# Performance work log

Measured on AMD Instinct MI355X. Metric: run time of the kernel, lower is better.

## Reference

```python
import jax, jax.numpy as jnp
import numpy as np

B, T, D, H, C = 64, 2048, 320, 256, 10  # batch, seq, input, hidden, classes


def _lstm_layer(x, W_ih, W_hh, b_ih, b_hh):
    """Single LSTM layer, batch_first x: [B,T,Din] -> [B,T,H].
    PyTorch gate order: i, f, g, o."""
    # Precompute input projections for all timesteps at once (big GEMM, efficient)
    xg = jnp.einsum('btd,gd->btg', x, W_ih) + b_ih + b_hh  # [B,T,4H]
    Hh = W_hh.shape[1]

    def step(carry, xt):
        h, c = carry
        g = xt + h @ W_hh.T  # [B,4H]
        i, f, gg, o = jnp.split(g, 4, axis=-1)
        i = jax.nn.sigmoid(i)
        f = jax.nn.sigmoid(f)
        gg = jnp.tanh(gg)
        o = jax.nn.sigmoid(o)
        c = f * c + i * gg
        h = o * jnp.tanh(c)
        return (h, c), h

    h0 = jnp.zeros((x.shape[0], Hh), x.dtype)
    (_, _), hs = jax.lax.scan(step, (h0, h0), jnp.swapaxes(xg, 0, 1))
    return jnp.swapaxes(hs, 0, 1)  # [B,T,H]


def setup_inputs() -> dict:
    key = jax.random.key(0)
    ks = jax.random.split(key, 12)
    s_ih0 = 1.0 / np.sqrt(H)
    inp = {
        'x': jax.random.normal(ks[0], (B, T, D), dtype=jnp.float32),
        'W_ih0': jax.random.uniform(ks[1], (4 * H, D), jnp.float32, -s_ih0, s_ih0),
        'W_hh0': jax.random.uniform(ks[2], (4 * H, H), jnp.float32, -s_ih0, s_ih0),
        'b_ih0': jax.random.uniform(ks[3], (4 * H,), jnp.float32, -s_ih0, s_ih0),
        'b_hh0': jax.random.uniform(ks[4], (4 * H,), jnp.float32, -s_ih0, s_ih0),
        'W_ih1': jax.random.uniform(ks[5], (4 * H, H), jnp.float32, -s_ih0, s_ih0),
        'W_hh1': jax.random.uniform(ks[6], (4 * H, H), jnp.float32, -s_ih0, s_ih0),
        'b_ih1': jax.random.uniform(ks[7], (4 * H,), jnp.float32, -s_ih0, s_ih0),
        'b_hh1': jax.random.uniform(ks[8], (4 * H,), jnp.float32, -s_ih0, s_ih0),
        'W_fc': jax.random.uniform(ks[9], (C, H), jnp.float32, -s_ih0, s_ih0),
        'b_fc': jax.random.uniform(ks[10], (C,), jnp.float32, -s_ih0, s_ih0),
    }
    return inp


def reference(x, W_ih0, W_hh0, b_ih0, b_hh0, W_ih1, W_hh1, b_ih1, b_hh1, W_fc, b_fc):
    h1 = _lstm_layer(x, W_ih0, W_hh0, b_ih0, b_hh0)   # [B,T,H]
    h2 = _lstm_layer(h1, W_ih1, W_hh1, b_ih1, b_hh1)  # [B,T,H]
    last = h2[:, -1, :]                                # output[:, -1, :]
    return last @ W_fc.T + b_fc                        # [B,C]
```

## Files before the change

### kernel.cpp

```cpp
#include <hip/hip_runtime.h>
#include <stdint.h>

typedef __bf16 bf16x8 __attribute__((ext_vector_type(8)));
typedef float f32x4 __attribute__((ext_vector_type(4)));
typedef unsigned long long u64;

#define BB 64
#define TT 2048
#define DD 320
#define HH 256
#define NC 10
#define GH 1024

#define GB 4
#define GJ 4
#define MB 16
#define JW 64
#define NTHREADS 512
#define SHS 264
#define SGS 260
#define NPAIR 2048
#define NPT 4
#define NRW 3
#define NWG_LAUNCH 64
#define HSROUNDS 3
#define HSSPIN 256

__device__ __forceinline__ unsigned short f2bf(float f) {
  unsigned u = __float_as_uint(f);
  u += 0x7FFF + ((u >> 16) & 1);
  return (unsigned short)(u >> 16);
}

__global__ void convert_bf16_k(const float* __restrict__ src,
                               unsigned short* __restrict__ dst, int n) {
  int i = blockIdx.x * blockDim.x + threadIdx.x;
  int st = gridDim.x * blockDim.x;
  for (; i < n; i += st) dst[i] = f2bf(src[i]);
}

__global__ void bias_sum_k(const float* __restrict__ a, const float* __restrict__ b,
                           float* __restrict__ d, int n) {
  int i = blockIdx.x * blockDim.x + threadIdx.x;
  if (i < n) d[i] = a[i] + b[i];
}

__global__ void zero_claim_k(int* p) { p[threadIdx.x] = 0; }

__device__ __forceinline__ float sigm(float x) { return 1.f / (1.f + __expf(-x)); }
__device__ __forceinline__ float tanh_s(float x) { return 2.f * sigm(2.f * x) - 1.f; }

__device__ __forceinline__ u64 ald(const u64* p) {
  return __hip_atomic_load(p, __ATOMIC_RELAXED, __HIP_MEMORY_SCOPE_AGENT);
}
__device__ __forceinline__ void ast(u64* p, u64 v) {
  __hip_atomic_store(p, v, __ATOMIC_RELAXED, __HIP_MEMORY_SCOPE_AGENT);
}

__device__ __forceinline__ void st_wt(u64* p, u64 v) {
  asm volatile("global_store_dwordx2 %0, %1, off" : : "v"(p), "v"(v) : "memory");
}
__device__ __forceinline__ void ld_sc0_issue(const u64* p, u64& d) {
  asm volatile("global_load_dwordx2 %0, %1, off sc0" : "=&v"(d) : "v"(p) : "memory");
}
__device__ __forceinline__ u64 ld1_sc0(const u64* p) {
  u64 v;
  asm volatile("global_load_dwordx2 %0, %1, off sc0\n\t"
               "s_waitcnt vmcnt(0)"
               : "=&v"(v) : "v"(p) : "memory");
  __builtin_amdgcn_sched_barrier(0);
  return v;
}
__device__ __forceinline__ void vm_wait0() {
  asm volatile("s_waitcnt vmcnt(0)" ::: "memory");
  __builtin_amdgcn_sched_barrier(0);
}

template <int KCX, bool IS_L0>
__device__ __forceinline__ void lstm_role(
    const unsigned short* __restrict__ xin,
    const u64* __restrict__ xtag,
    const unsigned short* __restrict__ Wih,
    const unsigned short* __restrict__ Whh,
    const float* __restrict__ bias,
    u64* __restrict__ h1out,
    float* __restrict__ hlast,
    u64* __restrict__ hx,
    unsigned short* sX, unsigned short* sH, float* sG,
    int gb, int gj, bool local)
{
  constexpr int KX = KCX * 32;
  constexpr int KCH = HH / 32;

  const int tid = threadIdx.x;
  const int wv = tid >> 6;
  const int ln = tid & 63;
  const int lm = ln & 15;
  const int lq = ln >> 4;
  const int j0 = gj * JW;
  const int b0 = gb * MB;

  bf16x8 bW[2][KCX + KCH];
  float bsv[2];
#pragma unroll
  for (int i = 0; i < 2; ++i) {
    int r = (wv * 2 + i) * 16 + lm;
    int grow = (r >> 6) * HH + j0 + (r & 63);
#pragma unroll
    for (int kc = 0; kc < KCX; ++kc)
      bW[i][kc] = *(const bf16x8*)&Wih[(size_t)grow * KX + kc * 32 + lq * 8];
#pragma unroll
    for (int kc = 0; kc < KCH; ++kc)
      bW[i][KCX + kc] = *(const bf16x8*)&Whh[(size_t)grow * HH + kc * 32 + lq * 8];
    bsv[i] = bias[grow];
  }

  int rw[NRW];
#pragma unroll
  for (int i = 0; i < NRW; ++i) {
    int rp = i * NTHREADS + tid;
    int em = rp / 96;
    int q = rp - em * 96;
    int pe = q >> 5;
    pe += (pe >= gj);
    rw[i] = em * 128 + pe * 32 + (q & 31);
  }

  u64* const hxg = hx + (size_t)gb * 2 * NPAIR;
  unsigned* const sHu = (unsigned*)sH;
  unsigned* const sXu = (unsigned*)sX;

  const int emb = tid >> 5;
  const int jp = tid & 31;
  const int jloc = jp * 2;
  const int wpair = emb * 128 + (j0 >> 1) + jp;
  float c0 = 0.f, c1 = 0.f;

  bf16x8 xf[IS_L0 ? KCX : 1];
  u64 qx[NPT];
  if (IS_L0) {
#pragma unroll
    for (int kc = 0; kc < KCX; ++kc)
      xf[kc] = *(const bf16x8*)&xin[((size_t)(b0 + lm) * TT + 0) * KX + kc * 32 + lq * 8];
  } else {
#pragma unroll
    for (int i = 0; i < NPT; ++i) {
      int w = i * NTHREADS + tid;
      const u64* p = &xtag[((size_t)(b0 + (w >> 7)) * TT + 0) * 128 + (w & 127)];
      if (local) ld_sc0_issue(p, qx[i]); else qx[i] = ald(p);
    }
  }

  __syncthreads();

#pragma unroll 1
  for (int t = 0; t < TT; ++t) {
    u64* const rb = hxg + (size_t)((t + 1) & 1) * NPAIR;
    u64 qh[NRW];
    if (t > 0) {
#pragma unroll
      for (int i = 0; i < NRW; ++i) {
        const u64* p = &rb[rw[i]];
        if (local) ld_sc0_issue(p, qh[i]); else qh[i] = ald(p);
      }
    }

    f32x4 ac[2][2] = {{{0.f, 0.f, 0.f, 0.f}, {0.f, 0.f, 0.f, 0.f}},
                      {{0.f, 0.f, 0.f, 0.f}, {0.f, 0.f, 0.f, 0.f}}};
    if (IS_L0) {
#pragma unroll
      for (int kc = 0; kc < KCX; ++kc) {
        ac[0][kc & 1] = __builtin_amdgcn_mfma_f32_16x16x32_bf16(xf[kc], bW[0][kc], ac[0][kc & 1], 0, 0, 0);
        ac[1][kc & 1] = __builtin_amdgcn_mfma_f32_16x16x32_bf16(xf[kc], bW[1][kc], ac[1][kc & 1], 0, 0, 0);
      }
    }
    if (local) vm_wait0();

    {
      const unsigned etx = (unsigned)(t + 1), eth = (unsigned)t;
      bool ok;
      do {
        bool okx = true, okh = true;
        if (!IS_L0) {
#pragma unroll
          for (int i = 0; i < NPT; ++i) okx &= ((unsigned)(qx[i] >> 32) == etx);
        }
        if (t > 0) {
#pragma unroll
          for (int i = 0; i < NRW; ++i) okh &= ((unsigned)(qh[i] >> 32) == eth);
        }
        ok = okx && okh;
        if (!ok) {
          if (!IS_L0 && !okx) {
#pragma unroll
            for (int i = 0; i < NPT; ++i) {
              int w = i * NTHREADS + tid;
              const u64* p = &xtag[((size_t)(b0 + (w >> 7)) * TT + t) * 128 + (w & 127)];
              if (local) ld_sc0_issue(p, qx[i]); else qx[i] = ald(p);
            }
          }
          if (t > 0 && !okh) {
#pragma unroll
            for (int i = 0; i < NRW; ++i) {
              const u64* p = &rb[rw[i]];
              if (local) ld_sc0_issue(p, qh[i]); else qh[i] = ald(p);
            }
          }
          if (local) vm_wait0();
        }
      } while (!ok);
    }

    if (!IS_L0) {
#pragma unroll
      for (int i = 0; i < NPT; ++i) {
        int w = i * NTHREADS + tid;
        sXu[(w >> 7) * (SHS / 2) + (w & 127)] = (unsigned)qx[i];
      }
    }
    if (t > 0) {
#pragma unroll
      for (int i = 0; i < NRW; ++i)
        sHu[(rw[i] >> 7) * (SHS / 2) + (rw[i] & 127)] = (unsigned)qh[i];
    }
    __syncthreads();

    if (t + 1 < TT) {
      if (IS_L0) {
#pragma unroll
        for (int kc = 0; kc < KCX; ++kc)
          xf[kc] = *(const bf16x8*)&xin[((size_t)(b0 + lm) * TT + (t + 1)) * KX + kc * 32 + lq * 8];
      } else {
#pragma unroll
        for (int i = 0; i < NPT; ++i) {
          int w = i * NTHREADS + tid;
          const u64* p = &xtag[((size_t)(b0 + (w >> 7)) * TT + (t + 1)) * 128 + (w & 127)];
          if (local) ld_sc0_issue(p, qx[i]); else qx[i] = ald(p);
        }
      }
    }

    if (!IS_L0) {
#pragma unroll
      for (int kc = 0; kc < KCX; ++kc) {
        bf16x8 a = *(const bf16x8*)&sX[lm * SHS + kc * 32 + lq * 8];
        ac[0][kc & 1] = __builtin_amdgcn_mfma_f32_16x16x32_bf16(a, bW[0][kc], ac[0][kc & 1], 0, 0, 0);
        ac[1][kc & 1] = __builtin_amdgcn_mfma_f32_16x16x32_bf16(a, bW[1][kc], ac[1][kc & 1], 0, 0, 0);
      }
    }
    if (t > 0) {
#pragma unroll
      for (int kc = 0; kc < KCH; ++kc) {
        bf16x8 a = *(const bf16x8*)&sH[lm * SHS + kc * 32 + lq * 8];
        ac[0][kc & 1] = __builtin_amdgcn_mfma_f32_16x16x32_bf16(a, bW[0][KCX + kc], ac[0][kc & 1], 0, 0, 0);
        ac[1][kc & 1] = __builtin_amdgcn_mfma_f32_16x16x32_bf16(a, bW[1][KCX + kc], ac[1][kc & 1], 0, 0, 0);
      }
    }

    f32x4 A0 = ac[0][0] + ac[0][1];
    f32x4 A1 = ac[1][0] + ac[1][1];
#pragma unroll
    for (int r = 0; r < 4; ++r) {
      sG[(lq * 4 + r) * SGS + (wv * 2 + 0) * 16 + lm] = A0[r] + bsv[0];
      sG[(lq * 4 + r) * SGS + (wv * 2 + 1) * 16 + lm] = A1[r] + bsv[1];
    }
    __syncthreads();

    {
      const float* gp = &sG[emb * SGS];
      float gi0 = gp[0 * JW + jloc], gi1 = gp[0 * JW + jloc + 1];
      float gf0 = gp[1 * JW + jloc], gf1 = gp[1 * JW + jloc + 1];
      float gg0 = gp[2 * JW + jloc], gg1 = gp[2 * JW + jloc + 1];
      float go0 = gp[3 * JW + jloc], go1 = gp[3 * JW + jloc + 1];
      c0 = sigm(gf0) * c0 + sigm(gi0) * tanh_s(gg0);
      c1 = sigm(gf1) * c1 + sigm(gi1) * tanh_s(gg1);
      float h0 = sigm(go0) * tanh_s(c0);
      float h1 = sigm(go1) * tanh_s(c1);
      unsigned pair = (unsigned)f2bf(h0) | ((unsigned)f2bf(h1) << 16);
      u64 val = ((u64)(unsigned)(t + 1) << 32) | pair;
      u64* pw = &hxg[(size_t)(t & 1) * NPAIR + wpair];
      if (local) st_wt(pw, val); else ast(pw, val);
      sHu[emb * (SHS / 2) + (j0 >> 1) + jp] = pair;
      if (IS_L0) {
        u64* po = &h1out[((size_t)(b0 + emb) * TT + t) * 128 + (j0 >> 1) + jp];
        if (local) st_wt(po, val); else ast(po, val);
      } else if (t == TT - 1) {
        hlast[(size_t)(b0 + emb) * HH + j0 + jloc] = h0;
        hlast[(size_t)(b0 + emb) * HH + j0 + jloc + 1] = h1;
      }
    }
  }
}

__launch_bounds__(NTHREADS, 1)
__global__ void lstm_fused(const unsigned short* __restrict__ xb,
                           u64* __restrict__ h1tag,
                           const unsigned short* __restrict__ Wih0,
                           const unsigned short* __restrict__ Whh0,
                           const float* __restrict__ bias0,
                           const unsigned short* __restrict__ Wih1,
                           const unsigned short* __restrict__ Whh1,
                           const float* __restrict__ bias1,
                           float* __restrict__ h2last,
                           u64* __restrict__ hx0, u64* __restrict__ hx1,
                           int* __restrict__ claim) {
  __shared__ __align__(16) unsigned short sX[MB * SHS];
  __shared__ __align__(16) unsigned short sH[MB * SHS];
  __shared__ __align__(16) float sG[MB * SGS];
  __shared__ int sCtl[2];

  const int gb = (int)blockIdx.x & 7;
  const int sub = (int)blockIdx.x >> 3;
  if (gb >= GB) return;

  if (threadIdx.x == 0) {
    u64* hs = (u64*)claim;
    unsigned* vd = (unsigned*)(claim + 64);
    const int gid = gb * 8 + sub;
    bool lok = true;
    for (int r = 0; r < HSROUNDS && lok; ++r) {
      st_wt(&hs[gid], ((u64)(0xC0DE0000u + (unsigned)r) << 32) | (unsigned)gid);
      int it = 0;
      bool all;
      do {
        all = true;
        for (int m = 0; m < 8; ++m) {
          u64 v = ld1_sc0(&hs[gb * 8 + m]);
          unsigned hv = (unsigned)(v >> 32) - 0xC0DE0000u;
          all &= (hv >= (unsigned)r && hv < (unsigned)HSROUNDS);
        }
      } while (!all && ++it < HSSPIN);
      lok &= all;
    }
    __hip_atomic_store(&vd[gid], lok ? 2u : 1u, __ATOMIC_RELAXED,
                       __HIP_MEMORY_SCOPE_AGENT);
    bool ul = true;
    for (int m = 0; m < 8; ++m) {
      unsigned v;
      do {
        v = __hip_atomic_load(&vd[gb * 8 + m], __ATOMIC_RELAXED,
                              __HIP_MEMORY_SCOPE_AGENT);
      } while (v == 0);
      ul &= (v == 2);
    }
    sCtl[0] = ul ? 1 : 0;
  }
  __syncthreads();
  const bool local = sCtl[0] != 0;

  const int role = sub >> 2;
  const int gj = sub & 3;
  if (role == 0)
    lstm_role<DD / 32, true>(xb, nullptr, Wih0, Whh0, bias0, h1tag, nullptr,
                             hx0, sX, sH, sG, gb, gj, local);
  else
    lstm_role<HH / 32, false>(nullptr, h1tag, Wih1, Whh1, bias1, nullptr,
                              h2last, hx1, sX, sH, sG, gb, gj, local);
}

__global__ void fc_k(const float* __restrict__ h, const float* __restrict__ W,
                     const float* __restrict__ b, float* __restrict__ out) {
  int tid = threadIdx.x;
  if (tid < BB * NC) {
    int bb = tid / NC, cc = tid % NC;
    float s = b[cc];
    for (int j = 0; j < HH; ++j) s += h[bb * HH + j] * W[cc * HH + j];
    out[tid] = s;
  }
}

extern "C" void kernel_launch(void* const* d_in, const int* in_sizes, int n_in,
                              void* d_out, int out_size, void* d_ws, size_t ws_size,
                              hipStream_t stream) {
  (void)in_sizes; (void)n_in; (void)out_size;
  const float* x    = (const float*)d_in[0];
  const float* Wih0 = (const float*)d_in[1];
  const float* Whh0 = (const float*)d_in[2];
  const float* bih0 = (const float*)d_in[3];
  const float* bhh0 = (const float*)d_in[4];
  const float* Wih1 = (const float*)d_in[5];
  const float* Whh1 = (const float*)d_in[6];
  const float* bih1 = (const float*)d_in[7];
  const float* bhh1 = (const float*)d_in[8];
  const float* Wfc  = (const float*)d_in[9];
  const float* bfc  = (const float*)d_in[10];

  char* p = (char*)d_ws;
  size_t off = 0;
  auto alloc = [&](size_t bytes) -> char* {
    char* q = p + off;
    off += (bytes + 255) & ~(size_t)255;
    return q;
  };
  u64* hx0 = (u64*)alloc((size_t)GB * 2 * NPAIR * 8);
  u64* hx1 = (u64*)alloc((size_t)GB * 2 * NPAIR * 8);
  float* bias0 = (float*)alloc(GH * 4);
  float* bias1 = (float*)alloc(GH * 4);
  unsigned short* Wih0b = (unsigned short*)alloc((size_t)GH * DD * 2);
  unsigned short* Whh0b = (unsigned short*)alloc((size_t)GH * HH * 2);
  unsigned short* Wih1b = (unsigned short*)alloc((size_t)GH * HH * 2);
  unsigned short* Whh1b = (unsigned short*)alloc((size_t)GH * HH * 2);
  float* h2last = (float*)alloc((size_t)BB * HH * 4);
  unsigned short* xb = (unsigned short*)alloc((size_t)BB * TT * DD * 2);
  u64* h1tag = (u64*)alloc((size_t)BB * TT * (HH / 2) * 8);
  int* claim = (int*)alloc(1024);

  if (ws_size < off) return;

  zero_claim_k<<<1, 256, 0, stream>>>(claim);
  convert_bf16_k<<<2048, 256, 0, stream>>>(x, xb, BB * TT * DD);
  convert_bf16_k<<<512, 256, 0, stream>>>(Wih0, Wih0b, GH * DD);
  convert_bf16_k<<<512, 256, 0, stream>>>(Whh0, Whh0b, GH * HH);
  convert_bf16_k<<<512, 256, 0, stream>>>(Wih1, Wih1b, GH * HH);
  convert_bf16_k<<<512, 256, 0, stream>>>(Whh1, Whh1b, GH * HH);
  bias_sum_k<<<4, 256, 0, stream>>>(bih0, bhh0, bias0, GH);
  bias_sum_k<<<4, 256, 0, stream>>>(bih1, bhh1, bias1, GH);
  lstm_fused<<<NWG_LAUNCH, NTHREADS, 0, stream>>>(
      xb, h1tag, Wih0b, Whh0b, bias0, Wih1b, Whh1b, bias1, h2last, hx0, hx1, claim);
  fc_k<<<1, 640, 0, stream>>>(h2last, Wfc, bfc, (float*)d_out);
}
```

Baseline: 7.206 ms.

## Replace LDS gate staging with in-register transpose and double-buffer shared tiles

Reorders the weight rows each wave holds so that one 4x4 transpose via lane shuffles puts the i, f, g, o gates of one (batch, hidden pair) into a single lane's accumulators. This removes the shared gate buffer and the second barrier per timestep. The X and H shared tiles are double-buffered by step parity, so each thread's own h write goes straight into the next step's buffer without a race. The price is extra shuffle instructions, twice the LDS for X and H, and a more complex mapping of lanes to output elements.

```diff
diff --git a/kernel.cpp b/kernel.cpp
--- a/kernel.cpp
+++ b/kernel.cpp
@@ -18,7 +18,6 @@
 #define JW 64
 #define NTHREADS 512
 #define SHS 264
-#define SGS 260
 #define NPAIR 2048
 #define NPT 4
 #define NRW 3
@@ -74,6 +73,28 @@
 __device__ __forceinline__ void vm_wait0() {
   asm volatile("s_waitcnt vmcnt(0)" ::: "memory");
   __builtin_amdgcn_sched_barrier(0);
+}
+
+__device__ __forceinline__ void xpose4(f32x4& v, int ln) {
+  const bool b0 = (ln & 1) != 0;
+  const bool b1 = (ln & 2) != 0;
+  float x0 = __shfl_xor((float)v[0], 1);
+  float x1 = __shfl_xor((float)v[1], 1);
+  float x2 = __shfl_xor((float)v[2], 1);
+  float x3 = __shfl_xor((float)v[3], 1);
+  f32x4 u;
+  u[0] = b0 ? x1 : v[0];
+  u[1] = b0 ? v[1] : x0;
+  u[2] = b0 ? x3 : v[2];
+  u[3] = b0 ? v[3] : x2;
+  float y0 = __shfl_xor((float)u[0], 2);
+  float y1 = __shfl_xor((float)u[1], 2);
+  float y2 = __shfl_xor((float)u[2], 2);
+  float y3 = __shfl_xor((float)u[3], 2);
+  v[0] = b1 ? y2 : u[0];
+  v[1] = b1 ? y3 : u[1];
+  v[2] = b1 ? u[2] : y0;
+  v[3] = b1 ? u[3] : y1;
 }
 
 template <int KCX, bool IS_L0>
@@ -86,7 +107,8 @@
     u64* __restrict__ h1out,
     float* __restrict__ hlast,
     u64* __restrict__ hx,
-    unsigned short* sX, unsigned short* sH, float* sG,
+    unsigned short* sX0, unsigned short* sX1,
+    unsigned short* sH0, unsigned short* sH1,
     int gb, int gj, bool local)
 {
   constexpr int KX = KCX * 32;
@@ -104,8 +126,7 @@
   float bsv[2];
 #pragma unroll
   for (int i = 0; i < 2; ++i) {
-    int r = (wv * 2 + i) * 16 + lm;
-    int grow = (r >> 6) * HH + j0 + (r & 63);
+    int grow = (lm & 3) * HH + j0 + wv * 8 + ((lm >> 2) << 1) + i;
 #pragma unroll
     for (int kc = 0; kc < KCX; ++kc)
       bW[i][kc] = *(const bf16x8*)&Wih[(size_t)grow * KX + kc * 32 + lq * 8];
@@ -127,13 +148,10 @@
   }
 
   u64* const hxg = hx + (size_t)gb * 2 * NPAIR;
-  unsigned* const sHu = (unsigned*)sH;
-  unsigned* const sXu = (unsigned*)sX;
-
-  const int emb = tid >> 5;
-  const int jp = tid & 31;
-  const int jloc = jp * 2;
-  const int wpair = emb * 128 + (j0 >> 1) + jp;
+
+  const int pbatch = lq * 4 + (lm & 3);
+  const int ppair  = wv * 4 + (lm >> 2);
+  const int wpair  = pbatch * 128 + (j0 >> 1) + ppair;
   float c0 = 0.f, c1 = 0.f;
 
   bf16x8 xf[IS_L0 ? KCX : 1];
@@ -155,6 +173,14 @@
 
 #pragma unroll 1
   for (int t = 0; t < TT; ++t) {
+    const int par = t & 1;
+    unsigned short* const sXc = par ? sX1 : sX0;
+    unsigned short* const sHc = par ? sH1 : sH0;
+    unsigned short* const sHn = par ? sH0 : sH1;
+    unsigned* const sXcu = (unsigned*)sXc;
+    unsigned* const sHcu = (unsigned*)sHc;
+    unsigned* const sHnu = (unsigned*)sHn;
+
     u64* const rb = hxg + (size_t)((t + 1) & 1) * NPAIR;
     u64 qh[NRW];
     if (t > 0) {
@@ -215,13 +241,13 @@
 #pragma unroll
       for (int i = 0; i < NPT; ++i) {
         int w = i * NTHREADS + tid;
-        sXu[(w >> 7) * (SHS / 2) + (w & 127)] = (unsigned)qx[i];
+        sXcu[(w >> 7) * (SHS / 2) + (w & 127)] = (unsigned)qx[i];
       }
     }
     if (t > 0) {
 #pragma unroll
       for (int i = 0; i < NRW; ++i)
-        sHu[(rw[i] >> 7) * (SHS / 2) + (rw[i] & 127)] = (unsigned)qh[i];
+        sHcu[(rw[i] >> 7) * (SHS / 2) + (rw[i] & 127)] = (unsigned)qh[i];
     }
     __syncthreads();
 
@@ -243,7 +269,7 @@
     if (!IS_L0) {
 #pragma unroll
       for (int kc = 0; kc < KCX; ++kc) {
-        bf16x8 a = *(const bf16x8*)&sX[lm * SHS + kc * 32 + lq * 8];
+        bf16x8 a = *(const bf16x8*)&sXc[lm * SHS + kc * 32 + lq * 8];
         ac[0][kc & 1] = __builtin_amdgcn_mfma_f32_16x16x32_bf16(a, bW[0][kc], ac[0][kc & 1], 0, 0, 0);
         ac[1][kc & 1] = __builtin_amdgcn_mfma_f32_16x16x32_bf16(a, bW[1][kc], ac[1][kc & 1], 0, 0, 0);
       }
@@ -251,7 +277,7 @@
     if (t > 0) {
 #pragma unroll
       for (int kc = 0; kc < KCH; ++kc) {
-        bf16x8 a = *(const bf16x8*)&sH[lm * SHS + kc * 32 + lq * 8];
+        bf16x8 a = *(const bf16x8*)&sHc[lm * SHS + kc * 32 + lq * 8];
         ac[0][kc & 1] = __builtin_amdgcn_mfma_f32_16x16x32_bf16(a, bW[0][KCX + kc], ac[0][kc & 1], 0, 0, 0);
         ac[1][kc & 1] = __builtin_amdgcn_mfma_f32_16x16x32_bf16(a, bW[1][KCX + kc], ac[1][kc & 1], 0, 0, 0);
       }
@@ -259,36 +285,27 @@
 
     f32x4 A0 = ac[0][0] + ac[0][1];
     f32x4 A1 = ac[1][0] + ac[1][1];
-#pragma unroll
-    for (int r = 0; r < 4; ++r) {
-      sG[(lq * 4 + r) * SGS + (wv * 2 + 0) * 16 + lm] = A0[r] + bsv[0];
-      sG[(lq * 4 + r) * SGS + (wv * 2 + 1) * 16 + lm] = A1[r] + bsv[1];
-    }
-    __syncthreads();
-
-    {
-      const float* gp = &sG[emb * SGS];
-      float gi0 = gp[0 * JW + jloc], gi1 = gp[0 * JW + jloc + 1];
-      float gf0 = gp[1 * JW + jloc], gf1 = gp[1 * JW + jloc + 1];
-      float gg0 = gp[2 * JW + jloc], gg1 = gp[2 * JW + jloc + 1];
-      float go0 = gp[3 * JW + jloc], go1 = gp[3 * JW + jloc + 1];
-      c0 = sigm(gf0) * c0 + sigm(gi0) * tanh_s(gg0);
-      c1 = sigm(gf1) * c1 + sigm(gi1) * tanh_s(gg1);
-      float h0 = sigm(go0) * tanh_s(c0);
-      float h1 = sigm(go1) * tanh_s(c1);
-      unsigned pair = (unsigned)f2bf(h0) | ((unsigned)f2bf(h1) << 16);
-      u64 val = ((u64)(unsigned)(t + 1) << 32) | pair;
-      u64* pw = &hxg[(size_t)(t & 1) * NPAIR + wpair];
-      if (local) st_wt(pw, val); else ast(pw, val);
-      sHu[emb * (SHS / 2) + (j0 >> 1) + jp] = pair;
-      if (IS_L0) {
-        u64* po = &h1out[((size_t)(b0 + emb) * TT + t) * 128 + (j0 >> 1) + jp];
-        if (local) st_wt(po, val); else ast(po, val);
-      } else if (t == TT - 1) {
-        hlast[(size_t)(b0 + emb) * HH + j0 + jloc] = h0;
-        hlast[(size_t)(b0 + emb) * HH + j0 + jloc + 1] = h1;
-      }
-    }
+    A0[0] += bsv[0]; A0[1] += bsv[0]; A0[2] += bsv[0]; A0[3] += bsv[0];
+    A1[0] += bsv[1]; A1[1] += bsv[1]; A1[2] += bsv[1]; A1[3] += bsv[1];
+    xpose4(A0, ln);
+    xpose4(A1, ln);
+
+    c0 = sigm(A0[1]) * c0 + sigm(A0[0]) * tanh_s(A0[2]);
+    c1 = sigm(A1[1]) * c1 + sigm(A1[0]) * tanh_s(A1[2]);
+    float h0 = sigm(A0[3]) * tanh_s(c0);
+    float h1 = sigm(A1[3]) * tanh_s(c1);
+    unsigned pair = (unsigned)f2bf(h0) | ((unsigned)f2bf(h1) << 16);
+    u64 val = ((u64)(unsigned)(t + 1) << 32) | pair;
+    u64* pw = &hxg[(size_t)par * NPAIR + wpair];
+    if (local) st_wt(pw, val); else ast(pw, val);
+    if (IS_L0) {
+      u64* po = &h1out[((size_t)(b0 + pbatch) * TT + t) * 128 + (j0 >> 1) + ppair];
+      if (local) st_wt(po, val); else ast(po, val);
+    } else if (t == TT - 1) {
+      hlast[(size_t)(b0 + pbatch) * HH + j0 + ppair * 2] = h0;
+      hlast[(size_t)(b0 + pbatch) * HH + j0 + ppair * 2 + 1] = h1;
+    }
+    sHnu[pbatch * (SHS / 2) + (j0 >> 1) + ppair] = pair;
   }
 }
 
@@ -304,9 +321,8 @@
                            float* __restrict__ h2last,
                            u64* __restrict__ hx0, u64* __restrict__ hx1,
                            int* __restrict__ claim) {
-  __shared__ __align__(16) unsigned short sX[MB * SHS];
-  __shared__ __align__(16) unsigned short sH[MB * SHS];
-  __shared__ __align__(16) float sG[MB * SGS];
+  __shared__ __align__(16) unsigned short sX[2][MB * SHS];
+  __shared__ __align__(16) unsigned short sH[2][MB * SHS];
   __shared__ int sCtl[2];
 
   const int gb = (int)blockIdx.x & 7;
@@ -352,10 +368,10 @@
   const int gj = sub & 3;
   if (role == 0)
     lstm_role<DD / 32, true>(xb, nullptr, Wih0, Whh0, bias0, h1tag, nullptr,
-                             hx0, sX, sH, sG, gb, gj, local);
+                             hx0, sX[0], sX[1], sH[0], sH[1], gb, gj, local);
   else
     lstm_role<HH / 32, false>(nullptr, h1tag, Wih1, Whh1, bias1, nullptr,
-                              h2last, hx1, sX, sH, sG, gb, gj, local);
+                              h2last, hx1, sX[0], sX[1], sH[0], sH[1], gb, gj, local);
 }
 
 __global__ void fc_k(const float* __restrict__ h, const float* __restrict__ W,
```

Result: slower. 10.68 ms (+48.2%).
